# Performance work log

Hardware: AMD Instinct MI355X
Metric: run time of the kernel (lower is better)

The kernel has to match this reference:

```python
import jax, jax.numpy as jnp
import numpy as np

T = 5       # fixed temporal factor in the original forward
HEADS = 8
DIM = 512
DIM_HEAD = 64
INNER = HEADS * DIM_HEAD  # 512 (must equal DIM for the masked scatter)


def setup_inputs() -> dict:
    key = jax.random.key(0)
    ks = jax.random.split(key, 8)
    bt, n = 40, 3137  # b=8, t=5; n-1 = 56*56 visual tokens
    x = jax.random.normal(ks[0], (bt, n, DIM), dtype=jnp.float32)
    mask = jax.random.randint(ks[1], (bt, 56, 56), 0, 2).astype(jnp.float32)
    s = 1.0 / np.sqrt(DIM)
    w_vq = jax.random.normal(ks[2], (DIM, INNER), dtype=jnp.float32) * s
    w_vkv = jax.random.normal(ks[3], (DIM, 2 * INNER), dtype=jnp.float32) * s
    w_aqkv = jax.random.normal(ks[4], (DIM, 3 * INNER), dtype=jnp.float32) * s
    w_out = jax.random.normal(ks[5], (INNER, DIM), dtype=jnp.float32) * s
    b_out = jnp.zeros((DIM,), dtype=jnp.float32)
    return {"x": x, "mask": mask, "w_vq": w_vq, "w_vkv": w_vkv,
            "w_aqkv": w_aqkv, "w_out": w_out, "b_out": b_out}


def reference(x, mask, w_vq, w_vkv, w_aqkv, w_out, b_out):
    bt, n, dim = x.shape
    b = bt // T
    nv = n - 1
    dh = DIM_HEAD
    scale = dh ** -0.5

    A = x[:, 0]        # (bt, dim) -- single 'action' token per frame
    V = x[:, 1:]       # (bt, nv, dim)
    m = mask.reshape(bt, nv, 1)

    aq, ak, av = jnp.split(A @ w_aqkv, 3, axis=-1)      # each (bt, INNER)
    vk, vv = jnp.split(V @ w_vkv, 2, axis=-1)           # each (bt, nv, INNER)
    vq = V @ w_vq                                        # (bt, nv, INNER)

    # --- A -> V cross attention: per batch, T A-queries over T*nv V keys ---
    qa = aq.reshape(b, T, HEADS, dh)
    Kv = vk.reshape(b, T * nv, HEADS, dh)
    Vv = vv.reshape(b, T * nv, HEADS, dh)
    av_dots = jnp.einsum('bqhd,bkhd->bhqk', qa, Kv) * scale
    av_attn = jax.nn.softmax(av_dots, axis=-1)
    av_o = jnp.einsum('bhqk,bkhd->bqhd', av_attn, Vv)   # (b, T, H, dh)
    a_out = av_o.reshape(bt, 1, INNER)

    # --- V -> A cross attention with block mask: every V token attends only
    # to its own batch's T A-tokens (the -inf block fill in the original) ---
    Qv = vq.reshape(b, T, nv, HEADS, dh)
    Ka = ak.reshape(b, T, HEADS, dh)
    Va = av.reshape(b, T, HEADS, dh)
    va_dots = jnp.einsum('bfnhd,bkhd->bhfnk', Qv, Ka) * scale
    va_attn = jax.nn.softmax(va_dots, axis=-1)          # softmax over T keys
    va_o = jnp.einsum('bhfnk,bkhd->bfnhd', va_attn, Va)
    v_full = va_o.reshape(bt, nv, INNER)

    # original: scatter attn out into V.clone() then * mask, under no_grad()
    # => masked positions get attention output, others V*0 = 0; detached.
    v_out = jax.lax.stop_gradient(v_full * m)

    out = jnp.concatenate([a_out, v_out], axis=1)       # (bt, n, INNER)
    return out @ w_out + b_out
```

## Files before the change

### kernel.cpp

```cpp
#include <hip/hip_runtime.h>

typedef unsigned short u16;
typedef unsigned int u32;
typedef __attribute__((ext_vector_type(8))) u16 u16x8;
typedef __attribute__((ext_vector_type(8))) __bf16 bf16x8;
typedef __attribute__((ext_vector_type(4))) float f32x4;

__device__ __forceinline__ float b2f(u16 u){ return __uint_as_float(((u32)u)<<16); }
__device__ __forceinline__ u16 f2b(float f){
  u32 b = __float_as_uint(f);
  return (u16)((b + 0x7fffu + ((b>>16)&1u))>>16);
}
__device__ __forceinline__ void gload16(const void* g, void* l){
  __builtin_amdgcn_global_load_lds((__attribute__((address_space(1))) void*)g,
                                   (__attribute__((address_space(3))) void*)l, 16, 0, 0);
}
__device__ __forceinline__ float wred_max(float v){
#pragma unroll
  for (int o=32;o>0;o>>=1) v = fmaxf(v, __shfl_xor(v,o));
  return v;
}
__device__ __forceinline__ float wred_sum(float v){
#pragma unroll
  for (int o=32;o>0;o>>=1) v += __shfl_xor(v,o);
  return v;
}

__global__ void k_cast_x(const float* __restrict__ x, u16* __restrict__ xb, int n8){
  int stride = gridDim.x*blockDim.x;
  for (int i = blockIdx.x*blockDim.x + threadIdx.x; i < n8; i += stride){
    const float4* p = (const float4*)(x + (size_t)i*8);
    float4 a = p[0], b = p[1];
    u16x8 o;
    o[0]=f2b(a.x); o[1]=f2b(a.y); o[2]=f2b(a.z); o[3]=f2b(a.w);
    o[4]=f2b(b.x); o[5]=f2b(b.y); o[6]=f2b(b.z); o[7]=f2b(b.w);
    *(u16x8*)(xb + (size_t)i*8) = o;
  }
}

__global__ void k_prep_w(const float* __restrict__ wvq, const float* __restrict__ wvkv,
                         const float* __restrict__ wout, u16* __restrict__ W1T,
                         u16* __restrict__ WoutT){
  int id = blockIdx.x*blockDim.x + threadIdx.x;
  if (id < 786432){
    int n = id >> 9, k = id & 511;
    float v = (n < 512) ? wvq[k*512 + n] : wvkv[k*1024 + (n-512)];
    W1T[id] = f2b(v);
  } else {
    int j = id - 786432;
    int n = j >> 9, k = j & 511;
    WoutT[j] = f2b(wout[k*512 + n]);
  }
}

__global__ void k_agent_qkv(const float* __restrict__ x, const float* __restrict__ w,
                            float* __restrict__ aqkv){
  int id = blockIdx.x*blockDim.x + threadIdx.x;
  int bt = id / 1536, c = id % 1536;
  const float* xr = x + (size_t)bt*3137*512;
  float s = 0.f;
  for (int k=0;k<512;k++) s += xr[k]*w[k*1536+c];
  aqkv[id] = s;
}

template<int FOUT>
__global__ __launch_bounds__(256) void k_gemm_bt(
    const u16* __restrict__ A, const u16* __restrict__ BT,
    int M, int N, int K,
    u16* __restrict__ Cb, float* __restrict__ Cf, const float* __restrict__ bias)
{
  __shared__ __align__(16) char Asm[128*64*2];
  __shared__ __align__(16) char Bsm[128*64*2];
  const int tid = threadIdx.x;
  const int wid = tid >> 6, lane = tid & 63;
  const int m0 = blockIdx.x * 128, n0 = blockIdx.y * 128;
  const char* Ab = (const char*)A;
  const char* Bb = (const char*)BT;
  size_t aoff[4], boff[4];
  int ldsoff[4];
#pragma unroll
  for (int i=0;i<4;i++){
    int L = i*4096 + wid*1024 + lane*16;
    int r = L >> 7;
    int cb = (L ^ ((r&7)<<4)) & 127;
    ldsoff[i] = i*4096 + wid*1024;
    int ra = m0 + r; if (ra >= M) ra = M-1;
    aoff[i] = (size_t)ra*(size_t)(K*2) + cb;
    boff[i] = (size_t)(n0 + r)*(size_t)(K*2) + cb;
  }
  f32x4 acc[4][4] = {};
  const int wm = (wid>>1)*64, wn = (wid&1)*64;

  for (int k0 = 0; k0 < K; k0 += 64){
#pragma unroll
    for (int i=0;i<4;i++){
      gload16(Ab + aoff[i] + k0*2, Asm + ldsoff[i]);
      gload16(Bb + boff[i] + k0*2, Bsm + ldsoff[i]);
    }
    __syncthreads();
#pragma unroll
    for (int kk=0;kk<2;kk++){
      const int cb = kk*64 + ((lane>>4)<<4);
      bf16x8 af[4], bfr[4];
#pragma unroll
      for (int mr=0;mr<4;mr++){
        int r = wm + mr*16 + (lane&15);
        af[mr] = *(const bf16x8*)(Asm + r*128 + (cb ^ ((r&7)<<4)));
      }
#pragma unroll
      for (int nc=0;nc<4;nc++){
        int r = wn + nc*16 + (lane&15);
        bfr[nc] = *(const bf16x8*)(Bsm + r*128 + (cb ^ ((r&7)<<4)));
      }
#pragma unroll
      for (int mr=0;mr<4;mr++)
#pragma unroll
        for (int nc=0;nc<4;nc++)
          acc[mr][nc] = __builtin_amdgcn_mfma_f32_16x16x32_bf16(af[mr], bfr[nc], acc[mr][nc], 0,0,0);
    }
    __syncthreads();
  }
#pragma unroll
  for (int mr=0;mr<4;mr++){
#pragma unroll
    for (int nc=0;nc<4;nc++){
#pragma unroll
      for (int rg=0;rg<4;rg++){
        int row = m0 + wm + mr*16 + ((lane>>4)<<2) + rg;
        int col = n0 + wn + nc*16 + (lane&15);
        if (row < M){
          float v = acc[mr][nc][rg];
          if (FOUT) Cf[(size_t)row*N + col] = v + bias[col];
          else      Cb[(size_t)row*N + col] = f2b(v);
        }
      }
    }
  }
}

__global__ __launch_bounds__(320) void k_attn_agent(
    const u16* __restrict__ out1, const float* __restrict__ aqkv,
    float* __restrict__ pm, float* __restrict__ pl, float* __restrict__ pacc)
{
  __shared__ __align__(16) char Ksm[16384];
  __shared__ __align__(16) char Vsm[16384];
  const int bid = blockIdx.x;
  const int sp = bid & 7, bh = bid >> 3, b = bh >> 3, h = bh & 7;
  const int tid = threadIdx.x, wid = tid >> 6, lane = tid & 63;
  const int q = wid;
  float qreg[64];
  {
    const float* ap = aqkv + ((size_t)(b*5+q)*1536 + h*64);
#pragma unroll
    for (int d=0; d<64; d++) qreg[d] = ap[d];
  }
  float m = -1e30f, l = 0.f;
  float acc[8] = {0,0,0,0,0,0,0,0};
  const int g0 = sp * 1960;
  for (int c = 0; c < 16; c++){
    for (int idx = tid; idx < 2048; idx += 320){
      int arr = idx >> 10, rem = idx & 1023;
      int r = rem >> 3, seg = rem & 7;
      int loc = c*128 + r; if (loc > 1959) loc = 1959;
      int gk = g0 + loc;
      int tk = gk / 3136, nv = gk - tk*3136;
      size_t grow = (size_t)((b*5+tk)*3137 + 1 + nv)*1536 + (arr ? 1024 : 512) + h*64 + seg*8;
      u16x8 v = *(const u16x8*)(out1 + grow);
      char* dst = arr ? Vsm : Ksm;
      *(u16x8*)(dst + r*128 + ((seg*16) ^ ((r&7)<<4))) = v;
    }
    __syncthreads();
    float s0 = 0.f, s1 = 0.f;
#pragma unroll
    for (int seg=0; seg<8; seg++){
      const int r0 = lane, r1 = 64 + lane;
      u16x8 k0 = *(const u16x8*)(Ksm + r0*128 + ((seg*16) ^ ((r0&7)<<4)));
      u16x8 k1 = *(const u16x8*)(Ksm + r1*128 + ((seg*16) ^ ((r1&7)<<4)));
#pragma unroll
      for (int j=0;j<8;j++){
        s0 += qreg[seg*8+j]*b2f(k0[j]);
        s1 += qreg[seg*8+j]*b2f(k1[j]);
      }
    }
    s0 *= 0.125f; s1 *= 0.125f;
    const int locbase = c*128;
    if (locbase + lane >= 1960)      s0 = -1e30f;
    if (locbase + 64 + lane >= 1960) s1 = -1e30f;
    float cmax = wred_max(fmaxf(s0, s1));
    float mn = fmaxf(m, cmax);
    float resc = __expf(m - mn);
    float p0 = (s0 > -1e29f) ? __expf(s0 - mn) : 0.f;
    float p1 = (s1 > -1e29f) ? __expf(s1 - mn) : 0.f;
    l = l*resc + wred_sum(p0 + p1);
#pragma unroll
    for (int j=0;j<8;j++) acc[j] *= resc;
    const int g = lane >> 3, cc = lane & 7;
#pragma unroll
    for (int i=0;i<16;i++){
      int k = i*8 + g;
      u16x8 vv = *(const u16x8*)(Vsm + k*128 + ((cc*16) ^ ((k&7)<<4)));
      float p = (i < 8) ? __shfl(p0, k) : __shfl(p1, k-64);
#pragma unroll
      for (int j=0;j<8;j++) acc[j] += p*b2f(vv[j]);
    }
    m = mn;
    __syncthreads();
  }
#pragma unroll
  for (int j=0;j<8;j++){
    float v = acc[j];
    v += __shfl_xor(v, 8); v += __shfl_xor(v, 16); v += __shfl_xor(v, 32);
    acc[j] = v;
  }
  const int base = (bh*8 + sp)*5 + q;
  if (lane == 0){ pm[base] = m; pl[base] = l; }
  if (lane < 8){
    float* pa = pacc + (size_t)base*64 + lane*8;
#pragma unroll
    for (int j=0;j<8;j++) pa[j] = acc[j];
  }
}

__global__ void k_agent_combine(const float* __restrict__ pm, const float* __restrict__ pl,
                                const float* __restrict__ pacc, u16* __restrict__ IN)
{
  const int id = blockIdx.x;
  const int q = id % 5, t2 = id / 5;
  const int h = t2 & 7, b = t2 >> 3;
  const int d = threadIdx.x;
  const int bh = b*8 + h;
  float ms = -1e30f;
#pragma unroll
  for (int s2=0;s2<8;s2++) ms = fmaxf(ms, pm[(bh*8+s2)*5+q]);
  float L = 0.f, o = 0.f;
#pragma unroll
  for (int s2=0;s2<8;s2++){
    int base = (bh*8+s2)*5+q;
    float w = __expf(pm[base]-ms);
    L += w*pl[base];
    o += w*pacc[(size_t)base*64 + d];
  }
  IN[(size_t)(b*5+q)*3137*512 + h*64 + d] = f2b(o / L);
}

__global__ __launch_bounds__(256) void k_attn_frame(
    const u16* __restrict__ out1, const float* __restrict__ aqkv,
    const float* __restrict__ mask, u16* __restrict__ IN)
{
  __shared__ float Ka[5][8][68];
  __shared__ float Va[5][8][68];
  const int b = blockIdx.y;
  const int tid = threadIdx.x;
  for (int i = tid; i < 2560; i += 256){
    int t = i >> 9, rem = i & 511, hh = rem >> 6, d = rem & 63;
    const float* src = aqkv + (size_t)(b*5+t)*1536;
    Ka[t][hh][d] = src[512 + hh*64 + d];
    Va[t][hh][d] = src[1024 + hh*64 + d];
  }
  __syncthreads();
  const int task = blockIdx.x*256 + tid;
  const int h = task & 7, rl = task >> 3;
  const int f = rl / 3136, nv = rl - f*3136;
  const int bt = b*5 + f;
  const size_t r1 = (size_t)bt*3137 + 1 + nv;
  const u16* qp = out1 + r1*1536 + h*64;
  float qf[64];
#pragma unroll
  for (int sg=0; sg<8; sg++){
    u16x8 v = *(const u16x8*)(qp + sg*8);
#pragma unroll
    for (int j=0;j<8;j++) qf[sg*8+j] = b2f(v[j]);
  }
  float sd[5];
#pragma unroll
  for (int t=0;t<5;t++){
    float s = 0.f;
#pragma unroll
    for (int d=0;d<64;d++) s += qf[d]*Ka[t][h][d];
    sd[t] = s*0.125f;
  }
  float mx = sd[0];
#pragma unroll
  for (int t=1;t<5;t++) mx = fmaxf(mx, sd[t]);
  float p[5], ps = 0.f;
#pragma unroll
  for (int t=0;t<5;t++){ p[t] = __expf(sd[t]-mx); ps += p[t]; }
  const float mv = mask[(size_t)bt*3136 + nv] / ps;
  u16* op = IN + r1*512 + h*64;
#pragma unroll
  for (int sg=0; sg<8; sg++){
    u16x8 o;
#pragma unroll
    for (int j=0;j<8;j++){
      const int d = sg*8+j;
      float v = 0.f;
#pragma unroll
      for (int t=0;t<5;t++) v += p[t]*Va[t][h][d];
      o[j] = f2b(v*mv);
    }
    *(u16x8*)(op + sg*8) = o;
  }
}

extern "C" void kernel_launch(void* const* d_in, const int* in_sizes, int n_in,
                              void* d_out, int out_size, void* d_ws, size_t ws_size,
                              hipStream_t stream)
{
  const float* x      = (const float*)d_in[0];
  const float* mask   = (const float*)d_in[1];
  const float* w_vq   = (const float*)d_in[2];
  const float* w_vkv  = (const float*)d_in[3];
  const float* w_aqkv = (const float*)d_in[4];
  const float* w_out  = (const float*)d_in[5];
  const float* b_out  = (const float*)d_in[6];
  float* out = (float*)d_out;
  char* ws = (char*)d_ws;

  constexpr size_t MR = 125480;
  constexpr size_t OFF_XB   = 0;
  constexpr size_t OFF_OUT1 = OFF_XB + MR*512*2;
  constexpr size_t OFF_W1T  = OFF_OUT1 + MR*1536*2;
  constexpr size_t OFF_WOT  = OFF_W1T + 1536*512*2;
  constexpr size_t OFF_AQKV = OFF_WOT + 512*512*2;
  constexpr size_t OFF_PM   = OFF_AQKV + 40*1536*4;
  constexpr size_t OFF_PL   = OFF_PM + 2560*4;
  constexpr size_t OFF_PACC = OFF_PL + 2560*4;

  u16* Xb     = (u16*)(ws + OFF_XB);
  u16* out1   = (u16*)(ws + OFF_OUT1);
  u16* W1T    = (u16*)(ws + OFF_W1T);
  u16* WoutT  = (u16*)(ws + OFF_WOT);
  float* aqkv = (float*)(ws + OFF_AQKV);
  float* pm   = (float*)(ws + OFF_PM);
  float* pl   = (float*)(ws + OFF_PL);
  float* pacc = (float*)(ws + OFF_PACC);

  k_cast_x<<<2048, 256, 0, stream>>>(x, Xb, 8030720);
  k_prep_w<<<4096, 256, 0, stream>>>(w_vq, w_vkv, w_out, W1T, WoutT);
  k_agent_qkv<<<240, 256, 0, stream>>>(x, w_aqkv, aqkv);
  k_gemm_bt<0><<<dim3(981,12), 256, 0, stream>>>(Xb, W1T, (int)MR, 1536, 512, out1, nullptr, nullptr);
  k_attn_agent<<<512, 320, 0, stream>>>(out1, aqkv, pm, pl, pacc);
  k_attn_frame<<<dim3(490,8), 256, 0, stream>>>(out1, aqkv, mask, Xb);
  k_agent_combine<<<320, 64, 0, stream>>>(pm, pl, pacc, Xb);
  k_gemm_bt<1><<<dim3(981,4), 256, 0, stream>>>(Xb, WoutT, (int)MR, 512, 512, nullptr, out, b_out);
}
```

Measured before the change: 823.2 us.

## Use 256x256 multi-stage pipelined GEMM and finer split for agent attention

Replaces the 128x128 single-buffered bf16 GEMM with a 256x256 tile, 512-thread kernel. It streams K in 32-wide slices through a 4-deep ring of LDS buffers, filled by direct global-to-LDS loads with explicit vmcnt waits, and stores operands in MFMA fragment order. It also raises wave priority around the MFMA block and uses nontemporal stores for outputs. Separately, the agent cross-attention split grows from 8 to 16 chunks per head for more parallelism, and its partial buffers are aliased onto the no-longer-needed W1T workspace. The 128KB LDS per block limits occupancy to one block per CU, and the aliasing relies on launch ordering.

Result: slower. 970.6 us (+17.9%).

```diff
diff --git a/kernel.cpp b/kernel.cpp
--- a/kernel.cpp
+++ b/kernel.cpp
@@ -64,64 +64,69 @@
 }
 
 template<int FOUT>
-__global__ __launch_bounds__(256) void k_gemm_bt(
+__global__ __launch_bounds__(512, 2) void k_gemm(
     const u16* __restrict__ A, const u16* __restrict__ BT,
     int M, int N, int K,
     u16* __restrict__ Cb, float* __restrict__ Cf, const float* __restrict__ bias)
 {
-  __shared__ __align__(16) char Asm[128*64*2];
-  __shared__ __align__(16) char Bsm[128*64*2];
+  __shared__ __align__(16) char Ls[4][32768];
   const int tid = threadIdx.x;
   const int wid = tid >> 6, lane = tid & 63;
-  const int m0 = blockIdx.x * 128, n0 = blockIdx.y * 128;
+  const int m0 = blockIdx.x * 256, n0 = blockIdx.y * 256;
+  const size_t K2 = (size_t)K * 2;
   const char* Ab = (const char*)A;
   const char* Bb = (const char*)BT;
-  size_t aoff[4], boff[4];
-  int ldsoff[4];
-#pragma unroll
-  for (int i=0;i<4;i++){
-    int L = i*4096 + wid*1024 + lane*16;
-    int r = L >> 7;
-    int cb = (L ^ ((r&7)<<4)) & 127;
-    ldsoff[i] = i*4096 + wid*1024;
-    int ra = m0 + r; if (ra >= M) ra = M-1;
-    aoff[i] = (size_t)ra*(size_t)(K*2) + cb;
-    boff[i] = (size_t)(n0 + r)*(size_t)(K*2) + cb;
-  }
-  f32x4 acc[4][4] = {};
-  const int wm = (wid>>1)*64, wn = (wid&1)*64;
-
-  for (int k0 = 0; k0 < K; k0 += 64){
-#pragma unroll
-    for (int i=0;i<4;i++){
-      gload16(Ab + aoff[i] + k0*2, Asm + ldsoff[i]);
-      gload16(Bb + boff[i] + k0*2, Bsm + ldsoff[i]);
-    }
-    __syncthreads();
-#pragma unroll
-    for (int kk=0;kk<2;kk++){
-      const int cb = kk*64 + ((lane>>4)<<4);
-      bf16x8 af[4], bfr[4];
-#pragma unroll
-      for (int mr=0;mr<4;mr++){
-        int r = wm + mr*16 + (lane&15);
-        af[mr] = *(const bf16x8*)(Asm + r*128 + (cb ^ ((r&7)<<4)));
-      }
-#pragma unroll
-      for (int nc=0;nc<4;nc++){
-        int r = wn + nc*16 + (lane&15);
-        bfr[nc] = *(const bf16x8*)(Bsm + r*128 + (cb ^ ((r&7)<<4)));
-      }
-#pragma unroll
-      for (int mr=0;mr<4;mr++)
-#pragma unroll
-        for (int nc=0;nc<4;nc++)
-          acc[mr][nc] = __builtin_amdgcn_mfma_f32_16x16x32_bf16(af[mr], bfr[nc], acc[mr][nc], 0,0,0);
-    }
-    __syncthreads();
-  }
-#pragma unroll
-  for (int mr=0;mr<4;mr++){
+  size_t asrc[2], bsrc[2];
+  const int ad0 = wid*1024, ad1 = 8192 + wid*1024;
+#pragma unroll
+  for (int i=0;i<2;i++){
+    int row = (i*8 + wid)*16 + (lane & 15);
+    int koff = (lane >> 4) << 4;
+    int ra = m0 + row; if (ra >= M) ra = M - 1;
+    asrc[i] = (size_t)ra * K2 + koff;
+    bsrc[i] = (size_t)(n0 + row) * K2 + koff;
+  }
+#define STAGEX(s4, ks) { \
+    size_t ko = (size_t)(ks) * 64; \
+    gload16(Ab + asrc[0] + ko, Ls[s4] + ad0); \
+    gload16(Ab + asrc[1] + ko, Ls[s4] + ad1); \
+    gload16(Bb + bsrc[0] + ko, Ls[s4] + 16384 + ad0); \
+    gload16(Bb + bsrc[1] + ko, Ls[s4] + 16384 + ad1); }
+
+  STAGEX(0, 0) STAGEX(1, 1) STAGEX(2, 2)
+  f32x4 acc[8][4] = {};
+  const int awb = (wid >> 2) * 8192;
+  const int bwb = 16384 + (wid & 3) * 4096;
+  const int NS = K >> 5;
+  int s4 = 0;
+  for (int ks = 0; ks < NS; ++ks){
+    const int pre = (ks + 3 < NS) ? ks + 3 : ks;
+    STAGEX((s4 + 3) & 3, pre)
+    asm volatile("s_waitcnt vmcnt(12)" ::: "memory");
+    __builtin_amdgcn_s_barrier();
+    const char* base = Ls[s4];
+    bf16x8 af[8], bfr[4];
+#pragma unroll
+    for (int mr=0;mr<8;mr++) af[mr] = *(const bf16x8*)(base + awb + mr*1024 + lane*16);
+#pragma unroll
+    for (int nc=0;nc<4;nc++) bfr[nc] = *(const bf16x8*)(base + bwb + nc*1024 + lane*16);
+    __builtin_amdgcn_sched_barrier(0);
+    asm volatile("s_waitcnt lgkmcnt(0)" ::: "memory");
+    __builtin_amdgcn_s_barrier();
+    __builtin_amdgcn_sched_barrier(0);
+    __builtin_amdgcn_s_setprio(1);
+#pragma unroll
+    for (int mr=0;mr<8;mr++)
+#pragma unroll
+      for (int nc=0;nc<4;nc++)
+        acc[mr][nc] = __builtin_amdgcn_mfma_f32_16x16x32_bf16(af[mr], bfr[nc], acc[mr][nc], 0,0,0);
+    __builtin_amdgcn_s_setprio(0);
+    s4 = (s4 + 1) & 3;
+  }
+#undef STAGEX
+  const int wm = (wid >> 2) * 128, wn = (wid & 3) * 64;
+#pragma unroll
+  for (int mr=0;mr<8;mr++){
 #pragma unroll
     for (int nc=0;nc<4;nc++){
 #pragma unroll
@@ -130,8 +135,8 @@
         int col = n0 + wn + nc*16 + (lane&15);
         if (row < M){
           float v = acc[mr][nc][rg];
-          if (FOUT) Cf[(size_t)row*N + col] = v + bias[col];
-          else      Cb[(size_t)row*N + col] = f2b(v);
+          if (FOUT) __builtin_nontemporal_store(v + bias[col], &Cf[(size_t)row*N + col]);
+          else      __builtin_nontemporal_store(f2b(v), &Cb[(size_t)row*N + col]);
         }
       }
     }
@@ -145,7 +150,7 @@
   __shared__ __align__(16) char Ksm[16384];
   __shared__ __align__(16) char Vsm[16384];
   const int bid = blockIdx.x;
-  const int sp = bid & 7, bh = bid >> 3, b = bh >> 3, h = bh & 7;
+  const int sp = bid & 15, bh = bid >> 4, b = bh >> 3, h = bh & 7;
   const int tid = threadIdx.x, wid = tid >> 6, lane = tid & 63;
   const int q = wid;
   float qreg[64];
@@ -156,12 +161,12 @@
   }
   float m = -1e30f, l = 0.f;
   float acc[8] = {0,0,0,0,0,0,0,0};
-  const int g0 = sp * 1960;
-  for (int c = 0; c < 16; c++){
+  const int g0 = sp * 980;
+  for (int c = 0; c < 8; c++){
     for (int idx = tid; idx < 2048; idx += 320){
       int arr = idx >> 10, rem = idx & 1023;
       int r = rem >> 3, seg = rem & 7;
-      int loc = c*128 + r; if (loc > 1959) loc = 1959;
+      int loc = c*128 + r; if (loc > 979) loc = 979;
       int gk = g0 + loc;
       int tk = gk / 3136, nv = gk - tk*3136;
       size_t grow = (size_t)((b*5+tk)*3137 + 1 + nv)*1536 + (arr ? 1024 : 512) + h*64 + seg*8;
@@ -184,8 +189,8 @@
     }
     s0 *= 0.125f; s1 *= 0.125f;
     const int locbase = c*128;
-    if (locbase + lane >= 1960)      s0 = -1e30f;
-    if (locbase + 64 + lane >= 1960) s1 = -1e30f;
+    if (locbase + lane >= 980)      s0 = -1e30f;
+    if (locbase + 64 + lane >= 980) s1 = -1e30f;
     float cmax = wred_max(fmaxf(s0, s1));
     float mn = fmaxf(m, cmax);
     float resc = __expf(m - mn);
@@ -212,7 +217,7 @@
     v += __shfl_xor(v, 8); v += __shfl_xor(v, 16); v += __shfl_xor(v, 32);
     acc[j] = v;
   }
-  const int base = (bh*8 + sp)*5 + q;
+  const int base = (bh*16 + sp)*5 + q;
   if (lane == 0){ pm[base] = m; pl[base] = l; }
   if (lane < 8){
     float* pa = pacc + (size_t)base*64 + lane*8;
@@ -231,11 +236,11 @@
   const int bh = b*8 + h;
   float ms = -1e30f;
 #pragma unroll
-  for (int s2=0;s2<8;s2++) ms = fmaxf(ms, pm[(bh*8+s2)*5+q]);
+  for (int s2=0;s2<16;s2++) ms = fmaxf(ms, pm[(bh*16+s2)*5+q]);
   float L = 0.f, o = 0.f;
 #pragma unroll
-  for (int s2=0;s2<8;s2++){
-    int base = (bh*8+s2)*5+q;
+  for (int s2=0;s2<16;s2++){
+    int base = (bh*16+s2)*5+q;
     float w = __expf(pm[base]-ms);
     L += w*pl[base];
     o += w*pacc[(size_t)base*64 + d];
@@ -322,9 +327,9 @@
   constexpr size_t OFF_W1T  = OFF_OUT1 + MR*1536*2;
   constexpr size_t OFF_WOT  = OFF_W1T + 1536*512*2;
   constexpr size_t OFF_AQKV = OFF_WOT + 512*512*2;
-  constexpr size_t OFF_PM   = OFF_AQKV + 40*1536*4;
-  constexpr size_t OFF_PL   = OFF_PM + 2560*4;
-  constexpr size_t OFF_PACC = OFF_PL + 2560*4;
+  constexpr size_t OFF_PM   = OFF_W1T;
+  constexpr size_t OFF_PL   = OFF_PM + 5120*4;
+  constexpr size_t OFF_PACC = OFF_PL + 5120*4;
 
   u16* Xb     = (u16*)(ws + OFF_XB);
   u16* out1   = (u16*)(ws + OFF_OUT1);
@@ -338,9 +343,9 @@
   k_cast_x<<<2048, 256, 0, stream>>>(x, Xb, 8030720);
   k_prep_w<<<4096, 256, 0, stream>>>(w_vq, w_vkv, w_out, W1T, WoutT);
   k_agent_qkv<<<240, 256, 0, stream>>>(x, w_aqkv, aqkv);
-  k_gemm_bt<0><<<dim3(981,12), 256, 0, stream>>>(Xb, W1T, (int)MR, 1536, 512, out1, nullptr, nullptr);
-  k_attn_agent<<<512, 320, 0, stream>>>(out1, aqkv, pm, pl, pacc);
+  k_gemm<0><<<dim3(491,6), 512, 0, stream>>>(Xb, W1T, (int)MR, 1536, 512, out1, nullptr, nullptr);
+  k_attn_agent<<<1024, 320, 0, stream>>>(out1, aqkv, pm, pl, pacc);
   k_attn_frame<<<dim3(490,8), 256, 0, stream>>>(out1, aqkv, mask, Xb);
   k_agent_combine<<<320, 64, 0, stream>>>(pm, pl, pacc, Xb);
-  k_gemm_bt<1><<<dim3(981,4), 256, 0, stream>>>(Xb, WoutT, (int)MR, 512, 512, nullptr, out, b_out);
-}
+  k_gemm<1><<<dim3(491,2), 512, 0, stream>>>(Xb, WoutT, (int)MR, 512, 512, nullptr, out, b_out);
+}
```
